# Performance work log

Measured on AMD Instinct MI355X. Metric: run time of the kernel, lower is better.

## Reference

```python
import jax, jax.numpy as jnp
import numpy as np

B, S, D, H = 4, 2048, 1024, 16  # batch, seq, n_embd, n_head
HD = D // H  # head size = 64


def setup_inputs() -> dict:
    key = jax.random.key(0)
    ks = jax.random.split(key, 5)
    s = 0.02
    return {
        "x": jax.random.normal(ks[0], (B, S, D), dtype=jnp.float32),
        "W_attn": jax.random.normal(ks[1], (D, 3 * D), dtype=jnp.float32) * s,
        "b_attn": jnp.zeros((3 * D,), dtype=jnp.float32),
        "W_proj": jax.random.normal(ks[2], (D, D), dtype=jnp.float32) * s,
        "b_proj": jnp.zeros((D,), dtype=jnp.float32),
    }


def reference(x, W_attn, b_attn, W_proj, b_proj):
    Bx, Sx, Dx = x.shape
    qkv = x @ W_attn + b_attn  # [B,S,3D]
    q, k, v = jnp.split(qkv, 3, axis=-1)
    # [B,H,S,hd]
    q = q.reshape(Bx, Sx, H, HD).transpose(0, 2, 1, 3)
    k = k.reshape(Bx, Sx, H, HD).transpose(0, 2, 1, 3)
    v = v.reshape(Bx, Sx, H, HD).transpose(0, 2, 1, 3)
    scale = 1.0 / jnp.sqrt(jnp.asarray(HD, dtype=x.dtype))
    att = jnp.einsum("bhqd,bhkd->bhqk", q, k) * scale  # [B,H,S,S]
    causal = jnp.tril(jnp.ones((Sx, Sx), dtype=bool))
    att = jnp.where(causal[None, None, :, :], att, jnp.asarray(-jnp.inf, dtype=att.dtype))
    att = jax.nn.softmax(att, axis=-1)
    y = jnp.einsum("bhqk,bhkd->bhqd", att, v)  # [B,H,S,hd]
    y = y.transpose(0, 2, 1, 3).reshape(Bx, Sx, Dx)
    return y @ W_proj + b_proj
```

## Files before the change

### kernel.cpp

```cpp
#include <hip/hip_runtime.h>
#include <math.h>

#define SEQ 2048
#define DIM 1024
#define NH 16
#define HD 64
#define QKV_LD 3072

typedef __attribute__((ext_vector_type(8))) __bf16 bf16x8;
typedef __attribute__((ext_vector_type(8))) unsigned short u16x8;
typedef __attribute__((ext_vector_type(4))) unsigned short u16x4;
typedef __attribute__((ext_vector_type(4))) float f32x4;

typedef unsigned int __attribute__((may_alias)) u32a;

__device__ __forceinline__ unsigned short f2b(float f) {
  unsigned int b = __builtin_bit_cast(unsigned int, f);
  return (unsigned short)((b + 0x7fffu + ((b >> 16) & 1u)) >> 16);
}

__device__ __forceinline__ void gload_lds16(const void* g, void* l) {
  __builtin_amdgcn_global_load_lds((const __attribute__((address_space(1))) void*)g,
                                   (__attribute__((address_space(3))) void*)l,
                                   16, 0, 0);
}

__device__ __forceinline__ bf16x8 ld_frag16(const unsigned short* p) {
  bf16x8 r;
  __builtin_memcpy(&r, __builtin_assume_aligned((void*)p, 16), 16);
  return r;
}

#define BARRIER_VM4()  asm volatile("s_waitcnt vmcnt(4)\ns_barrier" ::: "memory")
#define BARRIER_LGKM() asm volatile("s_waitcnt lgkmcnt(0)\ns_barrier" ::: "memory")
#define ISSUE_FENCE()  asm volatile("" ::: "memory")


__global__ void to_bf16_kernel(const float* __restrict__ x,
                               unsigned short* __restrict__ y, int n) {
  int i = (blockIdx.x * blockDim.x + threadIdx.x) * 4;
  if (i >= n) return;
  float4 v = *(const float4*)(x + i);
  u16x4 o;
  o.x = f2b(v.x); o.y = f2b(v.y); o.z = f2b(v.z); o.w = f2b(v.w);
  *(u16x4*)(y + i) = o;
}

__global__ void transpose_to_bf16_kernel(const float* __restrict__ W,
                                         unsigned short* __restrict__ WT,
                                         int K, int N) {
  __shared__ float tile[32][33];
  const int n0 = blockIdx.x * 32, k0 = blockIdx.y * 32;
  const int tx = threadIdx.x, ty = threadIdx.y;
  tile[ty][tx] = W[(size_t)(k0 + ty) * N + n0 + tx];
  __syncthreads();
  WT[(size_t)(n0 + ty) * K + k0 + tx] = f2b(tile[tx][ty]);
}


template <int OUT_F32>
__global__ __launch_bounds__(256, 2) void gemm_bt_kernel(
    const unsigned short* __restrict__ A,
    const unsigned short* __restrict__ BT,
    const float* __restrict__ bias,
    void* __restrict__ C, int M, int N, int K,
    int scale_cols, float scale_val) {
  __shared__ unsigned short As[128 * 32];
  __shared__ unsigned short Bs[128 * 32];

  const int tid = threadIdx.x;
  const int wave = tid >> 6;
  const int lane = tid & 63;
  const int quad = lane >> 4;
  const int l16 = lane & 15;
  const int m0 = blockIdx.y * 128;
  const int n0 = blockIdx.x * 128;
  const int wm = (wave >> 1) * 64;
  const int wn = (wave & 1) * 64;

  const size_t a_g = (size_t)(m0 + wave * 32 + (lane >> 2)) * K + (lane & 3) * 8;
  const size_t b_g = (size_t)(n0 + wave * 32 + (lane >> 2)) * K + (lane & 3) * 8;
  unsigned short* lA = As + wave * 1024;
  unsigned short* lB = Bs + wave * 1024;

  f32x4 acc[4][4] = {};

  for (int k0 = 0; k0 < K; k0 += 32) {
    gload_lds16(A + a_g + k0, lA);
    gload_lds16(A + a_g + (size_t)16 * K + k0, lA + 512);
    gload_lds16(BT + b_g + k0, lB);
    gload_lds16(BT + b_g + (size_t)16 * K + k0, lB + 512);
    __syncthreads();

    bf16x8 af[4], bfr[4];
#pragma unroll
    for (int i = 0; i < 4; ++i)
      af[i] = *(const bf16x8*)&As[(wm + i * 16 + l16) * 32 + quad * 8];
#pragma unroll
    for (int i = 0; i < 4; ++i)
      bfr[i] = *(const bf16x8*)&Bs[(wn + i * 16 + l16) * 32 + quad * 8];
#pragma unroll
    for (int mi = 0; mi < 4; ++mi)
#pragma unroll
      for (int ni = 0; ni < 4; ++ni)
        acc[mi][ni] = __builtin_amdgcn_mfma_f32_16x16x32_bf16(af[mi], bfr[ni],
                                                              acc[mi][ni], 0, 0, 0);
    __syncthreads();
  }

#pragma unroll
  for (int mi = 0; mi < 4; ++mi) {
#pragma unroll
    for (int ni = 0; ni < 4; ++ni) {
      const int col = n0 + wn + ni * 16 + l16;
      const int row = m0 + wm + mi * 16 + quad * 4;
      const float bv = bias[col];
      const float sv = (col < scale_cols) ? scale_val : 1.0f;
#pragma unroll
      for (int r = 0; r < 4; ++r) {
        float v = (acc[mi][ni][r] + bv) * sv;
        if (OUT_F32)
          ((float*)C)[(size_t)(row + r) * N + col] = v;
        else
          ((unsigned short*)C)[(size_t)(row + r) * N + col] = f2b(v);
      }
    }
  }
}


#define FA_PREFETCH(g_, via_, vib_)                                            \
  {                                                                            \
    const int _g = (g_);                                                       \
    const int _tg = (_g < ktA) ? _g : ((_g < 34) ? (_g - ktA) : 0);            \
    const unsigned short* _kg =                                                \
        base + (size_t)(_tg * 64 + ktok_l) * QKV_LD + DIM + h * HD + kchunk * 8; \
    gload_lds16(_kg, &Ks[_g % 3][0][w * 512]);                                 \
    gload_lds16(_kg + 32, &Ks[_g % 3][1][w * 512]);                            \
    const unsigned short* _vg =                                                \
        base + (size_t)(_tg * 64 + 2 * vk) * QKV_LD + 2 * DIM + h * HD + vc;   \
    via_ = *(const u16x8*)_vg;                                                 \
    vib_ = *(const u16x8*)(_vg + QKV_LD);                                      \
  }

#define VT_WRITE(va_, vb_)                                                     \
  {                                                                            \
    u32a* _V32 = (u32a*)Vt;                                                    \
    _Pragma("unroll") for (int j = 0; j < 8; ++j)                              \
      _V32[vwidx[j]] = (unsigned int)(va_)[j] | ((unsigned int)(vb_)[j] << 16);\
  }

#define FA_COMPUTE(i_, t_, kt_, qf_)                                           \
  {                                                                            \
    const unsigned short* _kb0 = &Ks[(i_) % 3][0][0];                          \
    const unsigned short* _kb1 = &Ks[(i_) % 3][1][0];                          \
    bf16x8 kf0[4], kf1[4], vf0[4], vf1[4];                                     \
    _Pragma("unroll") for (int ni = 0; ni < 4; ++ni) {                         \
      const int ro = (ni * 16 + l16) * 32 + ((quad ^ rsw) * 8);                \
      kf0[ni] = ld_frag16(_kb0 + ro);                                          \
      kf1[ni] = ld_frag16(_kb1 + ro);                                          \
      vf0[ni] = ld_frag16(&Vt[quad * 512 + vroff[ni]]);                        \
      vf1[ni] = ld_frag16(&Vt[(4 + quad) * 512 + vroff[ni]]);                  \
    }                                                                          \
    const int qloc = w * 16 + quad * 4;                                        \
    _Pragma("unroll") for (int m = 0; m < 2; ++m) {                            \
      if (!(m == 0 && (t_) == (kt_)-1)) {   \
        const bool diag = ((t_) == (kt_)-2 + m);                               \
        _Pragma("unroll") for (int ni = 0; ni < 4; ++ni) {                     \
          f32x4 a = {};                                                        \
          a = __builtin_amdgcn_mfma_f32_16x16x32_bf16(qf_[m][0], kf0[ni], a, 0, 0, 0); \
          a = __builtin_amdgcn_mfma_f32_16x16x32_bf16(qf_[m][1], kf1[ni], a, 0, 0, 0); \
          const int kloc = ni * 16 + l16;                                      \
          _Pragma("unroll") for (int r = 0; r < 4; ++r) {                      \
            float p = exp2f(a[r]);                                             \
            if (diag && kloc > qloc + r) p = 0.0f;                 \
            Ps[w][(quad * 4 + r) * 72 + kloc] =                                \
                (unsigned short)(__builtin_bit_cast(unsigned int, p) >> 16);   \
          }                                                                    \
        }                                                                      \
        _Pragma("unroll") for (int c = 0; c < 2; ++c) {                        \
          const bf16x8 pa = ld_frag16(&Ps[w][l16 * 72 + c * 32 + quad * 8]);   \
          _Pragma("unroll") for (int ni = 0; ni < 4; ++ni)                     \
            o[m][ni] = __builtin_amdgcn_mfma_f32_16x16x32_bf16(                \
                pa, c ? vf1[ni] : vf0[ni], o[m][ni], 0, 0, 0);                 \
          lacc[m] = __builtin_amdgcn_mfma_f32_16x16x32_bf16(pa, onesb,         \
                                                            lacc[m], 0, 0, 0);\
        }                                                                      \
      }                                                                        \
    }                                                                          \
  }

#define FA_ITER(i_, t_, kt_, qf_, pva, pvb, cva, cvb)                          \
  {                                                                            \
    FA_PREFETCH((i_) + 2, pva, pvb);                                           \
    FA_COMPUTE(i_, t_, kt_, qf_);                                              \
    BARRIER_VM4();                                                             \
    if ((i_) + 1 < 34) {                                                       \
      VT_WRITE(cva, cvb);                                                      \
      BARRIER_LGKM();                                                          \
    }                                                                          \
  }

#define FA_EPILOGUE(q0_)                                                       \
  _Pragma("unroll") for (int m = 0; m < 2; ++m)                                \
  _Pragma("unroll") for (int r = 0; r < 4; ++r) {                              \
    const float lv = __shfl(lacc[m][r], quad << 4);                            \
    const float inv = 1.0f / lv;                                               \
    const int row = (q0_) + m * 64 + w * 16 + quad * 4 + r;                    \
    unsigned short* dst = yatt + (size_t)(b * SEQ + row) * DIM + h * HD + l16; \
    _Pragma("unroll") for (int ni = 0; ni < 4; ++ni)                           \
      dst[ni * 16] = f2b(o[m][ni][r] * inv);                                   \
  }

__global__ __launch_bounds__(256, 2) void flash_kernel(
    const unsigned short* __restrict__ qkv,
    unsigned short* __restrict__ yatt) {
  __shared__ unsigned short Ks[3][2][64 * 32];
  __shared__ __align__(16) unsigned short Vt[8 * 64 * 8];
  __shared__ __align__(16) unsigned short Ps[4][16 * 72];

  const int tid = threadIdx.x;
  const int w = tid >> 6;
  const int lane = tid & 63;
  const int quad = lane >> 4;
  const int l16 = lane & 15;
  const int b = blockIdx.y >> 4;
  const int h = blockIdx.y & 15;
  const int jt = blockIdx.x;

  const unsigned short* base = qkv + (size_t)b * SEQ * QKV_LD;

  const int qtA = 15 - jt, qtB = jt;
  const int ktA = 2 * qtA + 2;
  const int ktB = 34 - ktA;
  const int q0A = qtA * 128, q0B = qtB * 128;

  const int ktok_l = w * 16 + (lane >> 2);
  const int ksw = (ktok_l ^ (ktok_l >> 2)) & 3;
  const int kchunk = (lane & 3) ^ ksw;
  const int rsw = (l16 ^ (l16 >> 2)) & 3;

  const int vk = tid >> 3;
  const int vc = (tid & 7) * 8;
  int vwidx[8];
#pragma unroll
  for (int j = 0; j < 8; ++j)
    vwidx[j] = (vk >> 2) * 256 + (vc | ((j + (vc >> 3)) & 7)) * 4 + (vk & 3);
  int vroff[4];
#pragma unroll
  for (int ni = 0; ni < 4; ++ni) {
    const int dim = ni * 16 + l16;
    vroff[ni] = ((dim & 56) | ((dim + (dim >> 3)) & 7)) * 8;
  }

  u16x8 ob = {};
  if (l16 == 0) {
#pragma unroll
    for (int j = 0; j < 8; ++j) ob[j] = 0x3F80;
  }
  const bf16x8 onesb = __builtin_bit_cast(bf16x8, ob);

  bf16x8 qfA[2][2], qfB[2][2];
#pragma unroll
  for (int m = 0; m < 2; ++m) {
    const unsigned short* qa =
        base + (size_t)(q0A + m * 64 + w * 16 + l16) * QKV_LD + h * HD + quad * 8;
    qfA[m][0] = *(const bf16x8*)qa;
    qfA[m][1] = *(const bf16x8*)(qa + 32);
    const unsigned short* qb =
        base + (size_t)(q0B + m * 64 + w * 16 + l16) * QKV_LD + h * HD + quad * 8;
    qfB[m][0] = *(const bf16x8*)qb;
    qfB[m][1] = *(const bf16x8*)(qb + 32);
  }

  u16x8 va0, vb0, va1, vb1;
  ISSUE_FENCE();
  FA_PREFETCH(0, va0, vb0);
  ISSUE_FENCE();
  FA_PREFETCH(1, va1, vb1);
  BARRIER_VM4();
  VT_WRITE(va0, vb0);
  BARRIER_LGKM();

  f32x4 o[2][4] = {};
  f32x4 lacc[2] = {};

  for (int i = 0; i < ktA; i += 2) {
    FA_ITER(i,     i,     ktA, qfA, va0, vb0, va1, vb1);
    FA_ITER(i + 1, i + 1, ktA, qfA, va1, vb1, va0, vb0);
  }
  FA_EPILOGUE(q0A);
#pragma unroll
  for (int m = 0; m < 2; ++m) {
    lacc[m] = (f32x4){};
#pragma unroll
    for (int ni = 0; ni < 4; ++ni) o[m][ni] = (f32x4){};
  }

  for (int i = ktA; i < 34; i += 2) {
    FA_ITER(i,     i - ktA,     ktB, qfB, va0, vb0, va1, vb1);
    FA_ITER(i + 1, i + 1 - ktA, ktB, qfB, va1, vb1, va0, vb0);
  }
  FA_EPILOGUE(q0B);
}


extern "C" void kernel_launch(void* const* d_in, const int* in_sizes, int n_in,
                              void* d_out, int out_size, void* d_ws, size_t ws_size,
                              hipStream_t stream) {
  const float* x  = (const float*)d_in[0];
  const float* Wa = (const float*)d_in[1];
  const float* ba = (const float*)d_in[2];
  const float* Wp = (const float*)d_in[3];
  const float* bp = (const float*)d_in[4];
  float* out = (float*)d_out;

  char* ws = (char*)d_ws;
  unsigned short* xb   = (unsigned short*)ws;
  unsigned short* WaT  = (unsigned short*)(ws + 16777216);
  unsigned short* WpT  = (unsigned short*)(ws + 23068672);
  unsigned short* qkv  = (unsigned short*)(ws + 25165824);
  unsigned short* yatt = (unsigned short*)(ws + 75497472);

  const int M = 4 * SEQ;
  const float qscale = 0.125f * 1.44269504089f;

  to_bf16_kernel<<<8192, 256, 0, stream>>>(x, xb, M * DIM);
  transpose_to_bf16_kernel<<<dim3(96, 32), dim3(32, 32), 0, stream>>>(Wa, WaT, DIM, 3 * DIM);
  transpose_to_bf16_kernel<<<dim3(32, 32), dim3(32, 32), 0, stream>>>(Wp, WpT, DIM, DIM);

  gemm_bt_kernel<0><<<dim3(24, 64), 256, 0, stream>>>(xb, WaT, ba, qkv, M, 3 * DIM, DIM,
                                                      DIM, qscale);

  flash_kernel<<<dim3(8, 4 * NH), 256, 0, stream>>>(qkv, yatt);

  gemm_bt_kernel<1><<<dim3(8, 64), 256, 0, stream>>>(yatt, WpT, bp, out, M, DIM, DIM,
                                                     0, 1.0f);
}
```

Baseline: 281.8 us.

## Split paired causal q-tiles into separate blocks, raise occupancy, use fast exp2

```diff
diff --git a/kernel.cpp b/kernel.cpp
--- a/kernel.cpp
+++ b/kernel.cpp
@@ -132,7 +132,7 @@
 #define FA_PREFETCH(g_, via_, vib_)                                            \
   {                                                                            \
     const int _g = (g_);                                                       \
-    const int _tg = (_g < ktA) ? _g : ((_g < 34) ? (_g - ktA) : 0);            \
+    const int _tg = (_g < kt) ? _g : 0;                                        \
     const unsigned short* _kg =                                                \
         base + (size_t)(_tg * 64 + ktok_l) * QKV_LD + DIM + h * HD + kchunk * 8; \
     gload_lds16(_kg, &Ks[_g % 3][0][w * 512]);                                 \
@@ -172,7 +172,7 @@
           a = __builtin_amdgcn_mfma_f32_16x16x32_bf16(qf_[m][1], kf1[ni], a, 0, 0, 0); \
           const int kloc = ni * 16 + l16;                                      \
           _Pragma("unroll") for (int r = 0; r < 4; ++r) {                      \
-            float p = exp2f(a[r]);                                             \
+            float p = __builtin_amdgcn_exp2f(a[r]);                            \
             if (diag && kloc > qloc + r) p = 0.0f;                 \
             Ps[w][(quad * 4 + r) * 72 + kloc] =                                \
                 (unsigned short)(__builtin_bit_cast(unsigned int, p) >> 16);   \
@@ -195,7 +195,7 @@
     FA_PREFETCH((i_) + 2, pva, pvb);                                           \
     FA_COMPUTE(i_, t_, kt_, qf_);                                              \
     BARRIER_VM4();                                                             \
-    if ((i_) + 1 < 34) {                                                       \
+    if ((i_) + 1 < (kt_)) {                                                    \
       VT_WRITE(cva, cvb);                                                      \
       BARRIER_LGKM();                                                          \
     }                                                                          \
@@ -212,7 +212,7 @@
       dst[ni * 16] = f2b(o[m][ni][r] * inv);                                   \
   }
 
-__global__ __launch_bounds__(256, 2) void flash_kernel(
+__global__ __launch_bounds__(256, 3) void flash_kernel(
     const unsigned short* __restrict__ qkv,
     unsigned short* __restrict__ yatt) {
   __shared__ unsigned short Ks[3][2][64 * 32];
@@ -226,14 +226,12 @@
   const int l16 = lane & 15;
   const int b = blockIdx.y >> 4;
   const int h = blockIdx.y & 15;
-  const int jt = blockIdx.x;
+
+  const int qt = 15 - (int)blockIdx.x;
+  const int kt = 2 * qt + 2;
+  const int q0 = qt * 128;
 
   const unsigned short* base = qkv + (size_t)b * SEQ * QKV_LD;
-
-  const int qtA = 15 - jt, qtB = jt;
-  const int ktA = 2 * qtA + 2;
-  const int ktB = 34 - ktA;
-  const int q0A = qtA * 128, q0B = qtB * 128;
 
   const int ktok_l = w * 16 + (lane >> 2);
   const int ksw = (ktok_l ^ (ktok_l >> 2)) & 3;
@@ -260,17 +258,13 @@
   }
   const bf16x8 onesb = __builtin_bit_cast(bf16x8, ob);
 
-  bf16x8 qfA[2][2], qfB[2][2];
+  bf16x8 qf[2][2];
 #pragma unroll
   for (int m = 0; m < 2; ++m) {
     const unsigned short* qa =
-        base + (size_t)(q0A + m * 64 + w * 16 + l16) * QKV_LD + h * HD + quad * 8;
-    qfA[m][0] = *(const bf16x8*)qa;
-    qfA[m][1] = *(const bf16x8*)(qa + 32);
-    const unsigned short* qb =
-        base + (size_t)(q0B + m * 64 + w * 16 + l16) * QKV_LD + h * HD + quad * 8;
-    qfB[m][0] = *(const bf16x8*)qb;
-    qfB[m][1] = *(const bf16x8*)(qb + 32);
+        base + (size_t)(q0 + m * 64 + w * 16 + l16) * QKV_LD + h * HD + quad * 8;
+    qf[m][0] = *(const bf16x8*)qa;
+    qf[m][1] = *(const bf16x8*)(qa + 32);
   }
 
   u16x8 va0, vb0, va1, vb1;
@@ -285,23 +279,11 @@
   f32x4 o[2][4] = {};
   f32x4 lacc[2] = {};
 
-  for (int i = 0; i < ktA; i += 2) {
-    FA_ITER(i,     i,     ktA, qfA, va0, vb0, va1, vb1);
-    FA_ITER(i + 1, i + 1, ktA, qfA, va1, vb1, va0, vb0);
-  }
-  FA_EPILOGUE(q0A);
-#pragma unroll
-  for (int m = 0; m < 2; ++m) {
-    lacc[m] = (f32x4){};
-#pragma unroll
-    for (int ni = 0; ni < 4; ++ni) o[m][ni] = (f32x4){};
-  }
-
-  for (int i = ktA; i < 34; i += 2) {
-    FA_ITER(i,     i - ktA,     ktB, qfB, va0, vb0, va1, vb1);
-    FA_ITER(i + 1, i + 1 - ktA, ktB, qfB, va1, vb1, va0, vb0);
-  }
-  FA_EPILOGUE(q0B);
+  for (int i = 0; i < kt; i += 2) {
+    FA_ITER(i,     i,     kt, qf, va0, vb0, va1, vb1);
+    FA_ITER(i + 1, i + 1, kt, qf, va1, vb1, va0, vb0);
+  }
+  FA_EPILOGUE(q0);
 }
 
 
@@ -332,7 +314,7 @@
   gemm_bt_kernel<0><<<dim3(24, 64), 256, 0, stream>>>(xb, WaT, ba, qkv, M, 3 * DIM, DIM,
                                                       DIM, qscale);
 
-  flash_kernel<<<dim3(8, 4 * NH), 256, 0, stream>>>(qkv, yatt);
+  flash_kernel<<<dim3(16, 4 * NH), 256, 0, stream>>>(qkv, yatt);
 
   gemm_bt_kernel<1><<<dim3(8, 64), 256, 0, stream>>>(yatt, WpT, bp, out, M, DIM, DIM,
                                                      0, 1.0f);
```

After: 309.2 us. +9.7%, slower.
